# Performance work log

Hardware: AMD Instinct MI355X
Metric: run time of the kernel (lower is better)

## Reference

```python
import jax, jax.numpy as jnp
import numpy as np

L = 128          # bandlimit (max_l)
NTHETA = 256     # Gauss-Legendre latitudes (>= L for exact quadrature)
NPHI = 512       # longitudes (>= 2L-1)
C_IN, C_OUT = 32, 32


def _normalized_assoc_legendre(Lmax, xg):
    """Pbar_lm(x) with Condon-Shortley phase, orthonormal on the sphere.
    Returns (Lmax, Lmax, T) for m>=0; zero for m>l."""
    T = xg.shape[0]
    P = np.zeros((Lmax, Lmax, T), dtype=np.float64)
    sx = np.sqrt(np.maximum(1.0 - xg * xg, 0.0))
    P[0, 0] = 1.0 / np.sqrt(4.0 * np.pi)
    for m in range(1, Lmax):
        P[m, m] = -np.sqrt((2 * m + 1) / (2.0 * m)) * sx * P[m - 1, m - 1]
    for m in range(0, Lmax - 1):
        P[m + 1, m] = np.sqrt(2 * m + 3.0) * xg * P[m, m]
    for m in range(Lmax):
        for l in range(m + 2, Lmax):
            a = np.sqrt((4.0 * l * l - 1.0) / (l * l - m * m))
            b = np.sqrt(((l - 1.0) ** 2 - m * m) / (4.0 * (l - 1.0) ** 2 - 1.0))
            P[l, m] = a * (xg * P[l - 1, m] - b * P[l - 2, m])
    return P


def _build_basis():
    # Gauss-Legendre quadrature in cos(theta): exact for degree <= 2*NTHETA-1
    xg, wg = np.polynomial.legendre.leggauss(NTHETA)
    P = _normalized_assoc_legendre(L, xg)  # (L, L, T), m>=0
    # Full basis B[l, m+L-1, t]; Pbar_{l,-m} = (-1)^m Pbar_{l,m}
    B = np.zeros((L, 2 * L - 1, NTHETA), dtype=np.float64)
    for m in range(-(L - 1), L):
        B[:, m + L - 1, :] = ((-1.0) ** abs(m) if m < 0 else 1.0) * P[:, abs(m), :]
    return B.astype(np.float32), wg.astype(np.float32)


def setup_inputs() -> dict:
    key = jax.random.key(0)
    k1, k2, k3 = jax.random.split(key, 3)
    x = jax.random.normal(k1, (NTHETA, NPHI, C_IN), dtype=jnp.float32)
    std = 1.0 / (C_IN + C_OUT)
    wr = std * jax.random.normal(k2, (L, 2 * L - 1, C_IN, C_OUT), dtype=jnp.float32)
    wi = std * jax.random.normal(k3, (L, 2 * L - 1, C_IN, C_OUT), dtype=jnp.float32)
    B, wg = _build_basis()
    return {"x": x, "weights_real": wr, "weights_imag": wi,
            "legendre": jnp.asarray(B), "quad_w": jnp.asarray(wg)}


def reference(x, weights_real, weights_imag, legendre, quad_w):
    ntheta, nphi, _ = x.shape
    Lb = legendre.shape[0]
    # --- forward SHT (per channel, vectorized) ---
    # longitude FFT: Fm[t,k,c] = sum_p x e^{-i 2pi k p / nphi}; dphi = 2pi/nphi
    Fm = jnp.fft.fft(x.astype(jnp.complex64), axis=1) * (2.0 * np.pi / nphi)
    midx = np.arange(-(Lb - 1), Lb) % nphi            # FFT bins for m=-(L-1)..L-1
    Fm_sel = Fm[:, midx, :]                           # (t, 2L-1, c)
    Bw = legendre * quad_w[None, None, :]             # quadrature-weighted basis
    # flm[l,m,c] = sum_t w_t Pbar_lm(theta_t) Fm[t,m,c]
    flm = jnp.einsum('lmt,tmc->lmc', Bw.astype(jnp.complex64), Fm_sel)
    # --- spectral conv: per-(l,m) channel mixing ---
    W = weights_real.astype(jnp.complex64) + 1j * weights_imag.astype(jnp.complex64)
    y = jnp.einsum('lmc,lmco->lmo', flm, W)           # (L, 2L-1, O)
    # --- inverse SHT ---
    G = jnp.einsum('lmt,lmo->tmo', legendre.astype(jnp.complex64), y)  # (t, 2L-1, O)
    spec = jnp.zeros((ntheta, nphi, G.shape[-1]), dtype=jnp.complex64)
    spec = spec.at[:, midx, :].set(G)
    out = jnp.fft.ifft(spec, axis=1) * nphi           # f = sum_m G e^{i m phi}
    return jnp.moveaxis(out.real, 2, 0)               # (O, ntheta, nphi)
```

## Files before the change

kernel.cpp:

```cpp
#include <hip/hip_runtime.h>
#include <math.h>

#define DEVFN __global__ __launch_bounds__(256)

namespace {
constexpr int LL  = 128;
constexpr int MM2 = 255;
constexpr int NT  = 256;
constexpr int NP  = 512;
constexpr int NC  = 32;
constexpr int NO  = 32;
constexpr float TWO_PI = 6.283185307179586476925286766559f;
}

typedef short v8s __attribute__((ext_vector_type(8)));
typedef float v4f __attribute__((ext_vector_type(4)));

__device__ inline unsigned short f2bf(float f) {
  unsigned int u = __float_as_uint(f);
  return (unsigned short)((u + 0x7FFFu + ((u >> 16) & 1u)) >> 16);
}

DEVFN void kp_prep(const float* __restrict__ x, unsigned short* __restrict__ tw1t,
                   unsigned short* __restrict__ vt, unsigned short* __restrict__ xb) {
  __shared__ float sm[32][65];
  const int bid = blockIdx.x;
  const int tid = threadIdx.x;
  const float phi = TWO_PI / (float)NP;
  if (bid < 512) {
    const int idx = bid * 256 + tid;
    const float fs = TWO_PI / (float)NP;
    {
      const int n = idx >> 9, p = idx & 511;
      const int m = n >> 1;
      const int k = (m * p) & (NP - 1);
      float s, c;
      sincosf(phi * (float)k, &s, &c);
      tw1t[idx] = f2bf((n & 1) ? (-s * fs) : (c * fs));
    }
    {
      const int p = idx >> 8, k = idx & 255;
      const int m = k >> 1;
      const int kk = (m * p) & (NP - 1);
      float s, c;
      sincosf(phi * (float)kk, &s, &c);
      vt[idx] = f2bf((k & 1) ? s : c);
    }
  } else {
    const int q = bid - 512;
    const int t = q >> 3;
    const int p0 = (q & 7) * 64;
#pragma unroll
    for (int i = 0; i < 8; ++i) {
      const int idx = tid + i * 256;
      const int p = idx >> 5, c = idx & 31;
      sm[c][p] = x[((size_t)t * NP + p0 + p) * NC + c];
    }
    __syncthreads();
    const int c = tid >> 3, pg = tid & 7;
    unsigned short pk[8];
#pragma unroll
    for (int u = 0; u < 8; ++u) pk[u] = f2bf(sm[c][pg * 8 + u]);
    *(uint4*)(xb + ((size_t)(t * 32 + c)) * NP + p0 + pg * 8) = *(const uint4*)pk;
  }
}

DEVFN void k1_mfma(const unsigned short* __restrict__ xb,
                   const unsigned short* __restrict__ tw1t,
                   const float* __restrict__ wg,
                   float* __restrict__ fwr, float* __restrict__ fwi) {
  __shared__ unsigned short As[128 * 32];
  __shared__ unsigned short Bs[64 * 32];
  const int tid = threadIdx.x;
  const int r0 = blockIdx.x * 128;
  const int n0 = blockIdx.y * 64;
  const int wid = tid >> 6, lane = tid & 63;
  const int wm = wid & 1, wn = wid >> 1;
  v4f acc[4][2];
#pragma unroll
  for (int i = 0; i < 4; ++i)
#pragma unroll
    for (int j = 0; j < 2; ++j) {
      acc[i][j][0] = 0.f; acc[i][j][1] = 0.f; acc[i][j][2] = 0.f; acc[i][j][3] = 0.f;
    }
  const int lr = lane & 15, lk = (lane >> 4) * 8;
  for (int k0 = 0; k0 < 512; k0 += 32) {
#pragma unroll
    for (int s = 0; s < 3; ++s) {
      const int chunk = tid + s * 256;
      if (chunk < 512) {
        const int row = chunk >> 2, c16 = chunk & 3;
        *(uint4*)&As[row * 32 + c16 * 8] =
            *(const uint4*)&xb[(size_t)(r0 + row) * 512 + k0 + c16 * 8];
      } else {
        const int bc = chunk - 512;
        const int row = bc >> 2, c16 = bc & 3;
        *(uint4*)&Bs[row * 32 + c16 * 8] =
            *(const uint4*)&tw1t[(size_t)(n0 + row) * 512 + k0 + c16 * 8];
      }
    }
    __syncthreads();
    v8s af[4], bf[2];
#pragma unroll
    for (int i = 0; i < 4; ++i) af[i] = *(const v8s*)&As[(wm * 64 + i * 16 + lr) * 32 + lk];
#pragma unroll
    for (int j = 0; j < 2; ++j) bf[j] = *(const v8s*)&Bs[(wn * 32 + j * 16 + lr) * 32 + lk];
#pragma unroll
    for (int i = 0; i < 4; ++i)
#pragma unroll
      for (int j = 0; j < 2; ++j)
        acc[i][j] = __builtin_amdgcn_mfma_f32_16x16x32_bf16(af[i], bf[j], acc[i][j], 0, 0, 0);
    __syncthreads();
  }
  const int lrow = (lane >> 4) * 4;
#pragma unroll
  for (int i = 0; i < 4; ++i) {
    const int rbase = r0 + wm * 64 + i * 16 + lrow;
    const int t = rbase >> 5, c0 = rbase & 31;
    const float w = wg[t];
#pragma unroll
    for (int j = 0; j < 2; ++j) {
      const int n = n0 + wn * 32 + j * 16 + lr;
      const int mI = n >> 1;
      float* dst = (n & 1) ? fwi : fwr;
      float4 v = {acc[i][j][0] * w, acc[i][j][1] * w, acc[i][j][2] * w, acc[i][j][3] * w};
      *(float4*)&dst[((size_t)mI * NT + t) * NC + c0] = v;
    }
  }
}

DEVFN void k23(const float* __restrict__ leg, const float* __restrict__ fwr,
               const float* __restrict__ fwi, const float* __restrict__ wr,
               const float* __restrict__ wi, float* __restrict__ ya,
               float* __restrict__ yb) {
  __shared__ float sf[4][64];
  const int fid  = blockIdx.x + (int)blockIdx.y * 128;
  const int wid4 = (fid & 7) * 512 + (fid >> 3);
  const int m  = wid4 >> 5;
  const int by = wid4 & 31;
  const int wid = threadIdx.x >> 6, lane = threadIdx.x & 63;
  const int l = m + by * 4 + wid;
  const bool valid = (l < LL);
  if (valid) {
    const int c = lane & 31;
    const float* lg = leg + ((size_t)(l * MM2 + 127 + m)) * NT;
    const float* fp = ((lane >> 5) ? fwi : fwr) + (size_t)m * NT * NC + c;
    float a = 0.f;
    for (int t = 0; t < NT; t += 4) {
      const float4 b4 = *(const float4*)(lg + t);
      a = fmaf(b4.x, fp[(t + 0) * NC], a);
      a = fmaf(b4.y, fp[(t + 1) * NC], a);
      a = fmaf(b4.z, fp[(t + 2) * NC], a);
      a = fmaf(b4.w, fp[(t + 3) * NC], a);
    }
    sf[wid][lane] = a;
  }
  __syncthreads();
  if (!valid) return;
  const int oo = lane & 31;
  const int half = lane >> 5;
  const float s0 = (m > 0) ? 1.0f : 0.0f;
  const size_t bp = ((size_t)(l * MM2 + 127 + m) * NC) * NO + oo;
  const size_t bn = ((size_t)(l * MM2 + 127 - m) * NC) * NO + oo;
  const float* fr = &sf[wid][half * 16];
  const float* fi = &sf[wid][32 + half * 16];
  float accA = 0.f, accB = 0.f;
#pragma unroll
  for (int u = 0; u < 16; ++u) {
    const size_t co = (size_t)(half * 16 + u) * NO;
    const float wrp = wr[bp + co];
    const float wrn = wr[bn + co];
    const float wip = wi[bp + co];
    const float win = wi[bn + co];
    const float fa = fr[u];
    const float fb = fi[u];
    const float wa = fmaf(s0, wrn, wrp);
    const float wb = fmaf(s0, win, -wip);
    accA = fmaf(fa, wa, fmaf(fb, wb, accA));
    accB = fmaf(fa, wb, fmaf(-fb, wa, accB));
  }
  accA += __shfl_down(accA, 32);
  accB += __shfl_down(accB, 32);
  if (lane < 32) {
    ya[(size_t)(m * LL + l) * NO + oo] = accA;
    yb[(size_t)(m * LL + l) * NO + oo] = accB;
  }
}

DEVFN void k4_G(const float* __restrict__ leg, const float* __restrict__ ya,
                const float* __restrict__ yb, unsigned short* __restrict__ ut) {
  const int fid  = blockIdx.x + (int)blockIdx.y * 128;
  const int wid4 = (fid & 7) * 128 + (fid >> 3);
  const int m = wid4 >> 3;
  const int o = threadIdx.x & 31;
  const int tq = threadIdx.x >> 5;
  const int t0 = (wid4 & 7) * 32 + tq * 4;
  float aa[4] = {}, bb[4] = {};
#pragma unroll 4
  for (int l = m; l < LL; ++l) {
    const float4 g = *(const float4*)(leg + ((size_t)(l * MM2 + 127 + m)) * NT + t0);
    const float yav = ya[(m * LL + l) * NO + o];
    const float ybv = yb[(m * LL + l) * NO + o];
    aa[0] = fmaf(g.x, yav, aa[0]);  bb[0] = fmaf(g.x, ybv, bb[0]);
    aa[1] = fmaf(g.y, yav, aa[1]);  bb[1] = fmaf(g.y, ybv, bb[1]);
    aa[2] = fmaf(g.z, yav, aa[2]);  bb[2] = fmaf(g.z, ybv, bb[2]);
    aa[3] = fmaf(g.w, yav, aa[3]);  bb[3] = fmaf(g.w, ybv, bb[3]);
  }
#pragma unroll
  for (int i = 0; i < 4; ++i) {
    const unsigned int pk = (unsigned int)f2bf(aa[i]) | ((unsigned int)f2bf(bb[i]) << 16);
    *(unsigned int*)&ut[((size_t)((t0 + i) * 32 + o)) * 256 + 2 * m] = pk;
  }
}

DEVFN void k5_mfma(const unsigned short* __restrict__ ut,
                   const unsigned short* __restrict__ vt,
                   float* __restrict__ out) {
  __shared__ unsigned short As[128 * 32];
  __shared__ unsigned short Bs[128 * 32];
  const int tid = threadIdx.x;
  const int p0 = blockIdx.x * 128;
  const int r0 = blockIdx.y * 128;
  const int wid = tid >> 6, lane = tid & 63;
  const int wm = wid & 1, wn = wid >> 1;
  v4f acc[4][4];
#pragma unroll
  for (int i = 0; i < 4; ++i)
#pragma unroll
    for (int j = 0; j < 4; ++j) {
      acc[i][j][0] = 0.f; acc[i][j][1] = 0.f; acc[i][j][2] = 0.f; acc[i][j][3] = 0.f;
    }
  const int lr = lane & 15, lk = (lane >> 4) * 8;
  for (int k0 = 0; k0 < 256; k0 += 32) {
#pragma unroll
    for (int s = 0; s < 2; ++s) {
      const int chunk = tid + s * 256;
      const int row = chunk >> 2, c16 = chunk & 3;
      *(uint4*)&As[row * 32 + c16 * 8] =
          *(const uint4*)&vt[(size_t)(p0 + row) * 256 + k0 + c16 * 8];
      *(uint4*)&Bs[row * 32 + c16 * 8] =
          *(const uint4*)&ut[(size_t)(r0 + row) * 256 + k0 + c16 * 8];
    }
    __syncthreads();
    v8s af[4], bf[4];
#pragma unroll
    for (int i = 0; i < 4; ++i) af[i] = *(const v8s*)&As[(wm * 64 + i * 16 + lr) * 32 + lk];
#pragma unroll
    for (int j = 0; j < 4; ++j) bf[j] = *(const v8s*)&Bs[(wn * 64 + j * 16 + lr) * 32 + lk];
#pragma unroll
    for (int i = 0; i < 4; ++i)
#pragma unroll
      for (int j = 0; j < 4; ++j)
        acc[i][j] = __builtin_amdgcn_mfma_f32_16x16x32_bf16(af[i], bf[j], acc[i][j], 0, 0, 0);
    __syncthreads();
  }
  const int lrow = (lane >> 4) * 4;
#pragma unroll
  for (int i = 0; i < 4; ++i) {
    const int pbase = p0 + wm * 64 + i * 16 + lrow;
#pragma unroll
    for (int j = 0; j < 4; ++j) {
      const int r = r0 + wn * 64 + j * 16 + lr;
      const int t = r >> 5, o = r & 31;
      float4 v = {acc[i][j][0], acc[i][j][1], acc[i][j][2], acc[i][j][3]};
      *(float4*)&out[((size_t)o * NT + t) * NP + pbase] = v;
    }
  }
}

extern "C" void kernel_launch(void* const* d_in, const int* in_sizes, int n_in,
                              void* d_out, int out_size, void* d_ws, size_t ws_size,
                              hipStream_t stream) {
  const float* x   = (const float*)d_in[0];
  const float* wr  = (const float*)d_in[1];
  const float* wi  = (const float*)d_in[2];
  const float* leg = (const float*)d_in[3];
  const float* wg  = (const float*)d_in[4];
  float* out = (float*)d_out;

  unsigned short* tw1t = (unsigned short*)d_ws;
  unsigned short* vt   = tw1t + 131072;
  unsigned short* xb   = vt + 131072;
  unsigned short* ut   = xb + 4194304;
  float* fwr = (float*)(ut + 2097152);
  float* fwi = fwr + 1048576;
  float* ya  = fwi + 1048576;
  float* yb  = ya + 524288;

  hipLaunchKernelGGL(kp_prep, dim3(2560), dim3(256), 0, stream, x, tw1t, vt, xb);
  hipLaunchKernelGGL(k1_mfma, dim3(64, 4), dim3(256), 0, stream, xb, tw1t, wg, fwr, fwi);
  hipLaunchKernelGGL(k23, dim3(128, 32), dim3(256), 0, stream, leg, fwr, fwi, wr, wi, ya, yb);
  hipLaunchKernelGGL(k4_G, dim3(128, 8), dim3(256), 0, stream, leg, ya, yb, ut);
  hipLaunchKernelGGL(k5_mfma, dim3(4, 64), dim3(256), 0, stream, ut, vt, out);
}
```

Measured before the change: 391.3 us.

## Compute four l-degrees per wave in k23 and balance m across XCDs

Each wave in k23 now computes four consecutive l values, so every load of the fw row is reused across four Legendre rows, and the grid shrinks fourfold. The m-to-block mapping in k23 and k4_G is changed to a zig-zag assignment (m_of) that pairs low and high m, spreading the triangular l>=m workload across the eight XCD groups. This adds register pressure and some clamped redundant loads for l past the end.

```diff
diff --git a/kernel.cpp b/kernel.cpp
--- a/kernel.cpp
+++ b/kernel.cpp
@@ -19,6 +19,10 @@
 __device__ inline unsigned short f2bf(float f) {
   unsigned int u = __float_as_uint(f);
   return (unsigned short)((u + 0x7FFFu + ((u >> 16) & 1u)) >> 16);
+}
+
+__device__ inline int m_of(int k, int mloc) {
+  return (mloc < 8) ? (8 * k + mloc) : (120 - 8 * k + (mloc - 8));
 }
 
 DEVFN void kp_prep(const float* __restrict__ x, unsigned short* __restrict__ tw1t,
@@ -129,72 +133,105 @@
   }
 }
 
-DEVFN void k23(const float* __restrict__ leg, const float* __restrict__ fwr,
-               const float* __restrict__ fwi, const float* __restrict__ wr,
-               const float* __restrict__ wi, float* __restrict__ ya,
-               float* __restrict__ yb) {
-  __shared__ float sf[4][64];
-  const int fid  = blockIdx.x + (int)blockIdx.y * 128;
-  const int wid4 = (fid & 7) * 512 + (fid >> 3);
-  const int m  = wid4 >> 5;
-  const int by = wid4 & 31;
+__global__ __launch_bounds__(256, 2) void k23(
+    const float* __restrict__ leg, const float* __restrict__ fwr,
+    const float* __restrict__ fwi, const float* __restrict__ wr,
+    const float* __restrict__ wi, float* __restrict__ ya,
+    float* __restrict__ yb) {
+  __shared__ float sf[4][4][64];
+  const int fid = blockIdx.x + (int)blockIdx.y * 128;
+  const int xk  = fid & 7;
+  const int loc = fid >> 3;
+  const int m   = m_of(xk, loc >> 3);
+  const int by  = loc & 7;
   const int wid = threadIdx.x >> 6, lane = threadIdx.x & 63;
-  const int l = m + by * 4 + wid;
-  const bool valid = (l < LL);
-  if (valid) {
+  const int lb  = m + by * 16 + wid * 4;
+  const bool wvalid = (lb < LL);
+  if (wvalid) {
     const int c = lane & 31;
-    const float* lg = leg + ((size_t)(l * MM2 + 127 + m)) * NT;
     const float* fp = ((lane >> 5) ? fwi : fwr) + (size_t)m * NT * NC + c;
-    float a = 0.f;
+    const int l0 = lb, l1 = min(lb + 1, LL - 1), l2 = min(lb + 2, LL - 1), l3 = min(lb + 3, LL - 1);
+    const float* lg0 = leg + ((size_t)(l0 * MM2 + 127 + m)) * NT;
+    const float* lg1 = leg + ((size_t)(l1 * MM2 + 127 + m)) * NT;
+    const float* lg2 = leg + ((size_t)(l2 * MM2 + 127 + m)) * NT;
+    const float* lg3 = leg + ((size_t)(l3 * MM2 + 127 + m)) * NT;
+    float a0 = 0.f, a1 = 0.f, a2 = 0.f, a3 = 0.f;
+#pragma unroll 2
     for (int t = 0; t < NT; t += 4) {
-      const float4 b4 = *(const float4*)(lg + t);
-      a = fmaf(b4.x, fp[(t + 0) * NC], a);
-      a = fmaf(b4.y, fp[(t + 1) * NC], a);
-      a = fmaf(b4.z, fp[(t + 2) * NC], a);
-      a = fmaf(b4.w, fp[(t + 3) * NC], a);
-    }
-    sf[wid][lane] = a;
+      const float f0 = fp[(t + 0) * NC];
+      const float f1 = fp[(t + 1) * NC];
+      const float f2 = fp[(t + 2) * NC];
+      const float f3 = fp[(t + 3) * NC];
+      const float4 b0 = *(const float4*)(lg0 + t);
+      const float4 b1 = *(const float4*)(lg1 + t);
+      const float4 b2 = *(const float4*)(lg2 + t);
+      const float4 b3 = *(const float4*)(lg3 + t);
+      a0 = fmaf(b0.x, f0, a0); a0 = fmaf(b0.y, f1, a0); a0 = fmaf(b0.z, f2, a0); a0 = fmaf(b0.w, f3, a0);
+      a1 = fmaf(b1.x, f0, a1); a1 = fmaf(b1.y, f1, a1); a1 = fmaf(b1.z, f2, a1); a1 = fmaf(b1.w, f3, a1);
+      a2 = fmaf(b2.x, f0, a2); a2 = fmaf(b2.y, f1, a2); a2 = fmaf(b2.z, f2, a2); a2 = fmaf(b2.w, f3, a2);
+      a3 = fmaf(b3.x, f0, a3); a3 = fmaf(b3.y, f1, a3); a3 = fmaf(b3.z, f2, a3); a3 = fmaf(b3.w, f3, a3);
+    }
+    sf[wid][0][lane] = a0;
+    sf[wid][1][lane] = a1;
+    sf[wid][2][lane] = a2;
+    sf[wid][3][lane] = a3;
   }
   __syncthreads();
-  if (!valid) return;
+  if (!wvalid) return;
   const int oo = lane & 31;
   const int half = lane >> 5;
   const float s0 = (m > 0) ? 1.0f : 0.0f;
-  const size_t bp = ((size_t)(l * MM2 + 127 + m) * NC) * NO + oo;
-  const size_t bn = ((size_t)(l * MM2 + 127 - m) * NC) * NO + oo;
-  const float* fr = &sf[wid][half * 16];
-  const float* fi = &sf[wid][32 + half * 16];
-  float accA = 0.f, accB = 0.f;
+  size_t bp[4], bn[4];
+#pragma unroll
+  for (int li = 0; li < 4; ++li) {
+    const int le = min(lb + li, LL - 1);
+    bp[li] = ((size_t)(le * MM2 + 127 + m) * NC) * NO + oo;
+    bn[li] = ((size_t)(le * MM2 + 127 - m) * NC) * NO + oo;
+  }
+  float accA[4] = {}, accB[4] = {};
 #pragma unroll
   for (int u = 0; u < 16; ++u) {
     const size_t co = (size_t)(half * 16 + u) * NO;
-    const float wrp = wr[bp + co];
-    const float wrn = wr[bn + co];
-    const float wip = wi[bp + co];
-    const float win = wi[bn + co];
-    const float fa = fr[u];
-    const float fb = fi[u];
-    const float wa = fmaf(s0, wrn, wrp);
-    const float wb = fmaf(s0, win, -wip);
-    accA = fmaf(fa, wa, fmaf(fb, wb, accA));
-    accB = fmaf(fa, wb, fmaf(-fb, wa, accB));
-  }
-  accA += __shfl_down(accA, 32);
-  accB += __shfl_down(accB, 32);
+#pragma unroll
+    for (int li = 0; li < 4; ++li) {
+      const float wrp = wr[bp[li] + co];
+      const float wrn = wr[bn[li] + co];
+      const float wip = wi[bp[li] + co];
+      const float win = wi[bn[li] + co];
+      const float fa = sf[wid][li][half * 16 + u];
+      const float fb = sf[wid][li][32 + half * 16 + u];
+      const float wa = fmaf(s0, wrn, wrp);
+      const float wb = fmaf(s0, win, -wip);
+      accA[li] = fmaf(fa, wa, fmaf(fb, wb, accA[li]));
+      accB[li] = fmaf(fa, wb, fmaf(-fb, wa, accB[li]));
+    }
+  }
+#pragma unroll
+  for (int li = 0; li < 4; ++li) {
+    accA[li] += __shfl_down(accA[li], 32);
+    accB[li] += __shfl_down(accB[li], 32);
+  }
   if (lane < 32) {
-    ya[(size_t)(m * LL + l) * NO + oo] = accA;
-    yb[(size_t)(m * LL + l) * NO + oo] = accB;
+#pragma unroll
+    for (int li = 0; li < 4; ++li) {
+      if (lb + li < LL) {
+        ya[(size_t)(m * LL + lb + li) * NO + oo] = accA[li];
+        yb[(size_t)(m * LL + lb + li) * NO + oo] = accB[li];
+      }
+    }
   }
 }
 
 DEVFN void k4_G(const float* __restrict__ leg, const float* __restrict__ ya,
                 const float* __restrict__ yb, unsigned short* __restrict__ ut) {
-  const int fid  = blockIdx.x + (int)blockIdx.y * 128;
-  const int wid4 = (fid & 7) * 128 + (fid >> 3);
-  const int m = wid4 >> 3;
+  const int fid = blockIdx.x + (int)blockIdx.y * 128;
+  const int xk  = fid & 7;
+  const int loc = fid >> 3;
+  const int m   = m_of(xk, loc >> 3);
+  const int tc  = loc & 7;
   const int o = threadIdx.x & 31;
   const int tq = threadIdx.x >> 5;
-  const int t0 = (wid4 & 7) * 32 + tq * 4;
+  const int t0 = tc * 32 + tq * 4;
   float aa[4] = {}, bb[4] = {};
 #pragma unroll 4
   for (int l = m; l < LL; ++l) {
@@ -289,7 +326,7 @@
 
   hipLaunchKernelGGL(kp_prep, dim3(2560), dim3(256), 0, stream, x, tw1t, vt, xb);
   hipLaunchKernelGGL(k1_mfma, dim3(64, 4), dim3(256), 0, stream, xb, tw1t, wg, fwr, fwi);
-  hipLaunchKernelGGL(k23, dim3(128, 32), dim3(256), 0, stream, leg, fwr, fwi, wr, wi, ya, yb);
+  hipLaunchKernelGGL(k23, dim3(128, 8), dim3(256), 0, stream, leg, fwr, fwi, wr, wi, ya, yb);
   hipLaunchKernelGGL(k4_G, dim3(128, 8), dim3(256), 0, stream, leg, ya, yb, ut);
   hipLaunchKernelGGL(k5_mfma, dim3(4, 64), dim3(256), 0, stream, ut, vt, out);
 }
```

Result: faster. 363.2 us (-7.2%).

## Split forward Legendre and channel mixing into separate kernels with vectorized mixing

Applied to the files above, without the earlier changes.

Splits the fused Legendre-projection and channel-mixing kernel into two kernels. The projection kernel computes two l rows per wave so each loaded Fm value is reused twice. The mixing kernel uses float4 weight loads over a 4x4 channel/output tile and finishes with xor-shuffle reductions. The G kernel also gets a new block-to-m mapping that pairs small and large m to balance the triangular work. In exchange this adds an extra kernel launch and an intermediate flm buffer round-trip through global memory.

```diff
diff --git a/kernel.cpp b/kernel.cpp
--- a/kernel.cpp
+++ b/kernel.cpp
@@ -19,6 +19,10 @@
 __device__ inline unsigned short f2bf(float f) {
   unsigned int u = __float_as_uint(f);
   return (unsigned short)((u + 0x7FFFu + ((u >> 16) & 1u)) >> 16);
+}
+
+__device__ inline int m_of(int k, int mloc) {
+  return (mloc < 8) ? (8 * k + mloc) : (120 - 8 * k + (mloc - 8));
 }
 
 DEVFN void kp_prep(const float* __restrict__ x, unsigned short* __restrict__ tw1t,
@@ -129,72 +133,99 @@
   }
 }
 
-DEVFN void k23(const float* __restrict__ leg, const float* __restrict__ fwr,
-               const float* __restrict__ fwi, const float* __restrict__ wr,
-               const float* __restrict__ wi, float* __restrict__ ya,
-               float* __restrict__ yb) {
-  __shared__ float sf[4][64];
-  const int fid  = blockIdx.x + (int)blockIdx.y * 128;
-  const int wid4 = (fid & 7) * 512 + (fid >> 3);
-  const int m  = wid4 >> 5;
-  const int by = wid4 & 31;
+DEVFN void k2_flm(const float* __restrict__ leg, const float* __restrict__ fwr,
+                  const float* __restrict__ fwi, float* __restrict__ flr,
+                  float* __restrict__ fli) {
+  const int m  = blockIdx.x;
+  const int l0 = m + blockIdx.y * 8 + (threadIdx.x >> 6) * 2;
+  if (l0 >= LL) return;
+  const int lane = threadIdx.x & 63;
+  const int c = lane & 31;
+  const int l1 = min(l0 + 1, LL - 1);
+  const float* fp = ((lane >> 5) ? fwi : fwr) + (size_t)m * NT * NC + c;
+  const float* lgA = leg + ((size_t)(l0 * MM2 + 127 + m)) * NT;
+  const float* lgB = leg + ((size_t)(l1 * MM2 + 127 + m)) * NT;
+  float a0 = 0.f, a1 = 0.f;
+#pragma unroll 4
+  for (int t = 0; t < NT; t += 4) {
+    const float f0 = fp[(t + 0) * NC];
+    const float f1 = fp[(t + 1) * NC];
+    const float f2 = fp[(t + 2) * NC];
+    const float f3 = fp[(t + 3) * NC];
+    const float4 bA = *(const float4*)(lgA + t);
+    const float4 bB = *(const float4*)(lgB + t);
+    a0 = fmaf(bA.x, f0, a0); a0 = fmaf(bA.y, f1, a0);
+    a0 = fmaf(bA.z, f2, a0); a0 = fmaf(bA.w, f3, a0);
+    a1 = fmaf(bB.x, f0, a1); a1 = fmaf(bB.y, f1, a1);
+    a1 = fmaf(bB.z, f2, a1); a1 = fmaf(bB.w, f3, a1);
+  }
+  float* outp = (lane >> 5) ? fli : flr;
+  outp[(size_t)(m * LL + l0) * NC + c] = a0;
+  if (l0 + 1 < LL) outp[(size_t)(m * LL + l0 + 1) * NC + c] = a1;
+}
+
+DEVFN void k3_mix(const float* __restrict__ flr, const float* __restrict__ fli,
+                  const float* __restrict__ wr, const float* __restrict__ wi,
+                  float* __restrict__ ya, float* __restrict__ yb) {
+  const int m  = blockIdx.x;
   const int wid = threadIdx.x >> 6, lane = threadIdx.x & 63;
-  const int l = m + by * 4 + wid;
-  const bool valid = (l < LL);
-  if (valid) {
-    const int c = lane & 31;
-    const float* lg = leg + ((size_t)(l * MM2 + 127 + m)) * NT;
-    const float* fp = ((lane >> 5) ? fwi : fwr) + (size_t)m * NT * NC + c;
-    float a = 0.f;
-    for (int t = 0; t < NT; t += 4) {
-      const float4 b4 = *(const float4*)(lg + t);
-      a = fmaf(b4.x, fp[(t + 0) * NC], a);
-      a = fmaf(b4.y, fp[(t + 1) * NC], a);
-      a = fmaf(b4.z, fp[(t + 2) * NC], a);
-      a = fmaf(b4.w, fp[(t + 3) * NC], a);
-    }
-    sf[wid][lane] = a;
-  }
-  __syncthreads();
-  if (!valid) return;
-  const int oo = lane & 31;
-  const int half = lane >> 5;
+  const int l = m + blockIdx.y * 4 + wid;
+  if (l >= LL) return;
+  const int c8 = lane >> 3;
+  const int o8 = lane & 7;
+  const int c0 = c8 * 4, o0 = o8 * 4;
   const float s0 = (m > 0) ? 1.0f : 0.0f;
-  const size_t bp = ((size_t)(l * MM2 + 127 + m) * NC) * NO + oo;
-  const size_t bn = ((size_t)(l * MM2 + 127 - m) * NC) * NO + oo;
-  const float* fr = &sf[wid][half * 16];
-  const float* fi = &sf[wid][32 + half * 16];
-  float accA = 0.f, accB = 0.f;
-#pragma unroll
-  for (int u = 0; u < 16; ++u) {
-    const size_t co = (size_t)(half * 16 + u) * NO;
-    const float wrp = wr[bp + co];
-    const float wrn = wr[bn + co];
-    const float wip = wi[bp + co];
-    const float win = wi[bn + co];
-    const float fa = fr[u];
-    const float fb = fi[u];
-    const float wa = fmaf(s0, wrn, wrp);
-    const float wb = fmaf(s0, win, -wip);
-    accA = fmaf(fa, wa, fmaf(fb, wb, accA));
-    accB = fmaf(fa, wb, fmaf(-fb, wa, accB));
-  }
-  accA += __shfl_down(accA, 32);
-  accB += __shfl_down(accB, 32);
-  if (lane < 32) {
-    ya[(size_t)(m * LL + l) * NO + oo] = accA;
-    yb[(size_t)(m * LL + l) * NO + oo] = accB;
+  const size_t rp = ((size_t)(l * MM2 + 127 + m) * NC) * NO;
+  const size_t rn = ((size_t)(l * MM2 + 127 - m) * NC) * NO;
+  const float4 fa4 = *(const float4*)&flr[(size_t)(m * LL + l) * NC + c0];
+  const float4 fb4 = *(const float4*)&fli[(size_t)(m * LL + l) * NC + c0];
+  float4 accA = {0.f, 0.f, 0.f, 0.f}, accB = {0.f, 0.f, 0.f, 0.f};
+#pragma unroll
+  for (int i = 0; i < 4; ++i) {
+    const int c = c0 + i;
+    const float4 wrp = *(const float4*)&wr[rp + (size_t)c * NO + o0];
+    const float4 wrn = *(const float4*)&wr[rn + (size_t)c * NO + o0];
+    const float4 wip = *(const float4*)&wi[rp + (size_t)c * NO + o0];
+    const float4 win = *(const float4*)&wi[rn + (size_t)c * NO + o0];
+    const float fa = (i == 0) ? fa4.x : (i == 1) ? fa4.y : (i == 2) ? fa4.z : fa4.w;
+    const float fb = (i == 0) ? fb4.x : (i == 1) ? fb4.y : (i == 2) ? fb4.z : fb4.w;
+    float4 wa, wb;
+    wa.x = fmaf(s0, wrn.x, wrp.x); wa.y = fmaf(s0, wrn.y, wrp.y);
+    wa.z = fmaf(s0, wrn.z, wrp.z); wa.w = fmaf(s0, wrn.w, wrp.w);
+    wb.x = fmaf(s0, win.x, -wip.x); wb.y = fmaf(s0, win.y, -wip.y);
+    wb.z = fmaf(s0, win.z, -wip.z); wb.w = fmaf(s0, win.w, -wip.w);
+    accA.x = fmaf(fa, wa.x, fmaf(fb, wb.x, accA.x));
+    accA.y = fmaf(fa, wa.y, fmaf(fb, wb.y, accA.y));
+    accA.z = fmaf(fa, wa.z, fmaf(fb, wb.z, accA.z));
+    accA.w = fmaf(fa, wa.w, fmaf(fb, wb.w, accA.w));
+    accB.x = fmaf(fa, wb.x, fmaf(-fb, wa.x, accB.x));
+    accB.y = fmaf(fa, wb.y, fmaf(-fb, wa.y, accB.y));
+    accB.z = fmaf(fa, wb.z, fmaf(-fb, wa.z, accB.z));
+    accB.w = fmaf(fa, wb.w, fmaf(-fb, wa.w, accB.w));
+  }
+#pragma unroll
+  for (int mask = 8; mask <= 32; mask <<= 1) {
+    accA.x += __shfl_xor(accA.x, mask); accA.y += __shfl_xor(accA.y, mask);
+    accA.z += __shfl_xor(accA.z, mask); accA.w += __shfl_xor(accA.w, mask);
+    accB.x += __shfl_xor(accB.x, mask); accB.y += __shfl_xor(accB.y, mask);
+    accB.z += __shfl_xor(accB.z, mask); accB.w += __shfl_xor(accB.w, mask);
+  }
+  if (c8 == 0) {
+    *(float4*)&ya[(size_t)(m * LL + l) * NO + o0] = accA;
+    *(float4*)&yb[(size_t)(m * LL + l) * NO + o0] = accB;
   }
 }
 
 DEVFN void k4_G(const float* __restrict__ leg, const float* __restrict__ ya,
                 const float* __restrict__ yb, unsigned short* __restrict__ ut) {
-  const int fid  = blockIdx.x + (int)blockIdx.y * 128;
-  const int wid4 = (fid & 7) * 128 + (fid >> 3);
-  const int m = wid4 >> 3;
+  const int fid = blockIdx.x + (int)blockIdx.y * 128;
+  const int xk  = fid & 7;
+  const int loc = fid >> 3;
+  const int m   = m_of(xk, loc >> 3);
+  const int tc  = loc & 7;
   const int o = threadIdx.x & 31;
   const int tq = threadIdx.x >> 5;
-  const int t0 = (wid4 & 7) * 32 + tq * 4;
+  const int t0 = tc * 32 + tq * 4;
   float aa[4] = {}, bb[4] = {};
 #pragma unroll 4
   for (int l = m; l < LL; ++l) {
@@ -284,12 +315,15 @@
   unsigned short* ut   = xb + 4194304;
   float* fwr = (float*)(ut + 2097152);
   float* fwi = fwr + 1048576;
-  float* ya  = fwi + 1048576;
+  float* flr = fwi + 1048576;
+  float* fli = flr + 524288;
+  float* ya  = fli + 524288;
   float* yb  = ya + 524288;
 
   hipLaunchKernelGGL(kp_prep, dim3(2560), dim3(256), 0, stream, x, tw1t, vt, xb);
   hipLaunchKernelGGL(k1_mfma, dim3(64, 4), dim3(256), 0, stream, xb, tw1t, wg, fwr, fwi);
-  hipLaunchKernelGGL(k23, dim3(128, 32), dim3(256), 0, stream, leg, fwr, fwi, wr, wi, ya, yb);
+  hipLaunchKernelGGL(k2_flm, dim3(128, 16), dim3(256), 0, stream, leg, fwr, fwi, flr, fli);
+  hipLaunchKernelGGL(k3_mix, dim3(128, 32), dim3(256), 0, stream, flr, fli, wr, wi, ya, yb);
   hipLaunchKernelGGL(k4_G, dim3(128, 8), dim3(256), 0, stream, leg, ya, yb, ut);
   hipLaunchKernelGGL(k5_mfma, dim3(4, 64), dim3(256), 0, stream, ut, vt, out);
 }
```

Measured after the change: 364.8 us. -6.8%, faster.
